# Kernel optimization log

Hardware: AMD Instinct MI355X
Metric: run time of the kernel (lower is better)

## Reference

```python
import jax, jax.numpy as jnp
import numpy as np

B, S, H, D = 8, 16, 32, 64
HID = H * D
PAST = 4096


def setup_inputs() -> dict:
    key = jax.random.key(0)
    ks = jax.random.split(key, 7)
    sc = 0.02
    return {
        "hidden_states": jax.random.normal(ks[0], (B, S, HID), jnp.float32),
        "past_k": jax.random.normal(ks[1], (B, H, PAST, D), jnp.float32),
        "past_v": jax.random.normal(ks[2], (B, H, PAST, D), jnp.float32),
        "wq": jax.random.normal(ks[3], (HID, HID), jnp.float32) * sc,
        "wk": jax.random.normal(ks[4], (HID, HID), jnp.float32) * sc,
        "wv": jax.random.normal(ks[5], (HID, HID), jnp.float32) * sc,
        "wo": jax.random.normal(ks[6], (HID, HID), jnp.float32) * sc,
    }


def reference(hidden_states, past_k, past_v, wq, wk, wv, wo):
    b, s, _ = hidden_states.shape
    # QKV projections (torch Linear: x @ W.T), split into heads -> [B,H,S,D]
    q = (hidden_states @ wq.T).reshape(b, s, H, D).transpose(0, 2, 1, 3)
    k = (hidden_states @ wk.T).reshape(b, s, H, D).transpose(0, 2, 1, 3)
    v = (hidden_states @ wv.T).reshape(b, s, H, D).transpose(0, 2, 1, 3)
    # KV-cache concat: [B,H,past+S,D]
    k = jnp.concatenate([past_k, k], axis=2)
    v = jnp.concatenate([past_v, v], axis=2)
    scale = 1.0 / jnp.sqrt(jnp.asarray(D, hidden_states.dtype))
    # scores [B,H,S,T]
    scores = jnp.einsum("bhsd,bhtd->bhst", q, k) * scale
    probs = jax.nn.softmax(scores, axis=-1)
    out = jnp.einsum("bhst,bhtd->bhsd", probs, v)
    out = out.transpose(0, 2, 1, 3).reshape(b, s, HID)
    return out @ wo.T
```

## Files before the change

kernel.cpp:

```cpp
#include <hip/hip_runtime.h>
#include <hip/hip_bf16.h>
#include <stdint.h>

#define HID 2048
#define NH  32
#define HD  64
#define NB  8
#define NS  16
#define PAST 4096

#define QSCALE 0.18033688011112042591f
#define MSTATIC 16.0f

typedef __attribute__((ext_vector_type(8))) short short8;
typedef __attribute__((ext_vector_type(4))) short short4v;
typedef __attribute__((ext_vector_type(4))) float f32x4;

#define MFMA(a, b, c) __builtin_amdgcn_mfma_f32_16x16x32_bf16((a), (b), (c), 0, 0, 0)

#define PART_STRIDE 1088
#define NSPLIT 8
#define MATSZ (128 * HID)
#define VP 68
#define WSLAB 4352

static __device__ __forceinline__ short f2bf(float f) {
    __hip_bfloat16 h = __float2bfloat16(f);
    return *reinterpret_cast<short*>(&h);
}

static __device__ __forceinline__ f32x4 ld4(const float* p) {
    return *reinterpret_cast<const f32x4*>(p);
}
static __device__ __forceinline__ f32x4 ldnt(const float* p) {
    return __builtin_nontemporal_load(reinterpret_cast<const f32x4*>(p));
}

static __device__ __forceinline__ short8 pack8(f32x4 a, f32x4 b) {
    short8 r;
    r[0] = f2bf(a[0]); r[1] = f2bf(a[1]); r[2] = f2bf(a[2]); r[3] = f2bf(a[3]);
    r[4] = f2bf(b[0]); r[5] = f2bf(b[1]); r[6] = f2bf(b[2]); r[7] = f2bf(b[3]);
    return r;
}

static __device__ __forceinline__ short4v pack4(f32x4 a) {
    short4v r;
    r[0] = f2bf(a[0]); r[1] = f2bf(a[1]); r[2] = f2bf(a[2]); r[3] = f2bf(a[3]);
    return r;
}

static __device__ __forceinline__ short8 pack8s(f32x4 a, f32x4 b, float s) {
    short8 r;
    r[0] = f2bf(a[0] * s); r[1] = f2bf(a[1] * s); r[2] = f2bf(a[2] * s); r[3] = f2bf(a[3] * s);
    r[4] = f2bf(b[0] * s); r[5] = f2bf(b[1] * s); r[6] = f2bf(b[2] * s); r[7] = f2bf(b[3] * s);
    return r;
}

__global__ __launch_bounds__(256) void cvt_kernel(const float* __restrict__ in,
                                                  short* __restrict__ out) {
    int i = (blockIdx.x * 256 + threadIdx.x) * 4;
    f32x4 v = ld4(in + i);
    *reinterpret_cast<short4v*>(out + i) = pack4(v);
}

__global__ __launch_bounds__(128) void proj_kernel(
        const short* __restrict__ X,
        const float* __restrict__ W0, const float* __restrict__ W1,
        const float* __restrict__ W2,
        float* __restrict__ Yp) {
    int mat   = blockIdx.x >> 9;
    int rest  = blockIdx.x & 511;
    int strip = rest >> 2, ks = rest & 3;
    int nbase = strip * 16;
    int k0    = ks * 512;
    const float* W = (mat == 0) ? W0 : (mat == 1) ? W1 : W2;
    float* Y = Yp + (size_t)(mat * 4 + ks) * MATSZ;

    int lane = threadIdx.x & 63;
    int wave = threadIdx.x >> 6;
    int lr = lane & 15, g = lane >> 4;

    f32x4 acc0 = {0.f, 0.f, 0.f, 0.f};
    f32x4 acc1 = {0.f, 0.f, 0.f, 0.f};
    f32x4 acc2 = {0.f, 0.f, 0.f, 0.f};
    f32x4 acc3 = {0.f, 0.f, 0.f, 0.f};

    const short* xr = X + (size_t)(wave * 64 + lr) * HID + g * 8 + k0;
    const float* wr = W + (size_t)(nbase + lr) * HID + g * 8 + k0;

    #pragma unroll 4
    for (int kc = 0; kc < 512; kc += 32) {
        f32x4 w0 = ldnt(wr + kc);
        f32x4 w1 = ldnt(wr + kc + 4);
        short8 bb = pack8(w0, w1);
        short8 a0 = *reinterpret_cast<const short8*>(xr + kc);
        short8 a1 = *reinterpret_cast<const short8*>(xr + (size_t)16 * HID + kc);
        short8 a2 = *reinterpret_cast<const short8*>(xr + (size_t)32 * HID + kc);
        short8 a3 = *reinterpret_cast<const short8*>(xr + (size_t)48 * HID + kc);
        acc0 = MFMA(a0, bb, acc0);
        acc1 = MFMA(a1, bb, acc1);
        acc2 = MFMA(a2, bb, acc2);
        acc3 = MFMA(a3, bb, acc3);
    }
    #define STACC(accv, f) do { \
        Y[(size_t)(wave * 64 + (f) * 16 + (g << 2) + 0) * HID + nbase + lr] = accv[0]; \
        Y[(size_t)(wave * 64 + (f) * 16 + (g << 2) + 1) * HID + nbase + lr] = accv[1]; \
        Y[(size_t)(wave * 64 + (f) * 16 + (g << 2) + 2) * HID + nbase + lr] = accv[2]; \
        Y[(size_t)(wave * 64 + (f) * 16 + (g << 2) + 3) * HID + nbase + lr] = accv[3]; \
    } while (0)
    STACC(acc0, 0); STACC(acc1, 1); STACC(acc2, 2); STACC(acc3, 3);
    #undef STACC
}

__global__ __launch_bounds__(256) void merge4_kernel(
        const float* __restrict__ Yp,
        float* __restrict__ Y0, float* __restrict__ Y1, float* __restrict__ Y2) {
    int mat = blockIdx.x >> 8;
    int blk = blockIdx.x & 255;
    float* Y = (mat == 0) ? Y0 : (mat == 1) ? Y1 : Y2;
    const float* P = Yp + (size_t)mat * 4 * MATSZ;
    int idx = blk * 1024 + threadIdx.x * 4;
    f32x4 a = ld4(P + idx);
    f32x4 b = ld4(P + MATSZ + idx);
    f32x4 c = ld4(P + 2 * MATSZ + idx);
    f32x4 d = ld4(P + 3 * MATSZ + idx);
    f32x4 s = a + b + c + d;
    *reinterpret_cast<f32x4*>(Y + idx) = s;
}

__global__ __launch_bounds__(256, 4) void attn_kernel(
        const float* __restrict__ q,
        const float* __restrict__ knew, const float* __restrict__ vnew,
        const float* __restrict__ pastK, const float* __restrict__ pastV,
        float* __restrict__ parts) {
    __shared__ __align__(16) unsigned char lds_raw[4 * WSLAB];
    __shared__ float s_l[4][4][16];

    int bid = blockIdx.x;
    int bh = bid >> 3, split = bid & 7;
    int b = bh >> 5, h = bh & 31;
    int wave = threadIdx.x >> 6, lane = threadIdx.x & 63;
    int lq = lane & 15, g = lane >> 4;
    int vrow = lane >> 4;
    int vcol = (lane & 15) * 4;

    unsigned short* vbuf0 = (unsigned short*)(lds_raw + wave * WSLAB);
    unsigned short* vbuf1 = vbuf0 + 16 * VP;

    const float* qp = q + (size_t)(b * NS + lq) * HID + h * HD + g * 8;
    short8 qf0, qf1;
    {
        f32x4 a0 = ld4(qp);
        f32x4 a1 = ld4(qp + 4);
        f32x4 a2 = ld4(qp + 32);
        f32x4 a3 = ld4(qp + 36);
        qf0 = pack8s(a0, a1, QSCALE);
        qf1 = pack8s(a2, a3, QSCALE);
    }

    f32x4 o0 = {0.f, 0.f, 0.f, 0.f};
    f32x4 o1 = {0.f, 0.f, 0.f, 0.f};
    f32x4 o2 = {0.f, 0.f, 0.f, 0.f};
    f32x4 o3 = {0.f, 0.f, 0.f, 0.f};
    float lsum = 0.0f;

    const float* ksplit = pastK + (size_t)bh * PAST * HD + (size_t)split * 512 * HD;
    const float* vsplit = pastV + (size_t)bh * PAST * HD + (size_t)split * 512 * HD;

    #define ISSUE_K(T, A, Bv, C, D) do { \
        const float* kr_ = ksplit + (size_t)((T) * 64 + wave * 16 + lq) * HD + (g << 3); \
        A  = ldnt(kr_); \
        Bv = ldnt(kr_ + 4); \
        C  = ldnt(kr_ + 32); \
        D  = ldnt(kr_ + 36); \
    } while (0)

    #define ISSUE_V(T, V0, V1, V2, V3) do { \
        const float* vr_ = vsplit + (size_t)((T) * 64 + wave * 16) * HD; \
        V0 = ldnt(vr_ + (0 * 4 + vrow) * HD + vcol); \
        V1 = ldnt(vr_ + (1 * 4 + vrow) * HD + vcol); \
        V2 = ldnt(vr_ + (2 * 4 + vrow) * HD + vcol); \
        V3 = ldnt(vr_ + (3 * 4 + vrow) * HD + vcol); \
    } while (0)

    #define DSW(V0, V1, V2, V3, BUFP) do { \
        unsigned short* ds_ = (BUFP); \
        *reinterpret_cast<short4v*>(ds_ + (0 * 4 + vrow) * VP + vcol) = pack4(V0); \
        *reinterpret_cast<short4v*>(ds_ + (1 * 4 + vrow) * VP + vcol) = pack4(V1); \
        *reinterpret_cast<short4v*>(ds_ + (2 * 4 + vrow) * VP + vcol) = pack4(V2); \
        *reinterpret_cast<short4v*>(ds_ + (3 * 4 + vrow) * VP + vcol) = pack4(V3); \
    } while (0)

    #define QKSM(A, Bv, C, D, PF) do { \
        short8 af0 = pack8(A, Bv); \
        short8 af1 = pack8(C, D); \
        f32x4 sv = {0.f, 0.f, 0.f, 0.f}; \
        sv = MFMA(af0, qf0, sv); \
        sv = MFMA(af1, qf1, sv); \
        float e0 = exp2f(sv[0] - MSTATIC); \
        float e1 = exp2f(sv[1] - MSTATIC); \
        float e2 = exp2f(sv[2] - MSTATIC); \
        float e3 = exp2f(sv[3] - MSTATIC); \
        lsum += e0 + e1 + e2 + e3; \
        PF[0] = f2bf(e0); PF[1] = f2bf(e1); PF[2] = f2bf(e2); PF[3] = f2bf(e3); \
        PF[4] = 0; PF[5] = 0; PF[6] = 0; PF[7] = 0; \
    } while (0)

    #define PV(BUFP, PF) do { \
        const unsigned short* vc = (BUFP) + (g << 2) * VP; \
        short8 vf; \
        vf[4] = 0; vf[5] = 0; vf[6] = 0; vf[7] = 0; \
        vf[0] = (short)vc[0 * VP + lq];      vf[1] = (short)vc[1 * VP + lq]; \
        vf[2] = (short)vc[2 * VP + lq];      vf[3] = (short)vc[3 * VP + lq]; \
        o0 = MFMA(vf, PF, o0); \
        vf[0] = (short)vc[0 * VP + 16 + lq]; vf[1] = (short)vc[1 * VP + 16 + lq]; \
        vf[2] = (short)vc[2 * VP + 16 + lq]; vf[3] = (short)vc[3 * VP + 16 + lq]; \
        o1 = MFMA(vf, PF, o1); \
        vf[0] = (short)vc[0 * VP + 32 + lq]; vf[1] = (short)vc[1 * VP + 32 + lq]; \
        vf[2] = (short)vc[2 * VP + 32 + lq]; vf[3] = (short)vc[3 * VP + 32 + lq]; \
        o2 = MFMA(vf, PF, o2); \
        vf[0] = (short)vc[0 * VP + 48 + lq]; vf[1] = (short)vc[1 * VP + 48 + lq]; \
        vf[2] = (short)vc[2 * VP + 48 + lq]; vf[3] = (short)vc[3 * VP + 48 + lq]; \
        o3 = MFMA(vf, PF, o3); \
    } while (0)

    f32x4 kA0, kA1, kA2, kA3, kB0, kB1, kB2, kB3;
    f32x4 vA0, vA1, vA2, vA3, vB0, vB1, vB2, vB3;

    ISSUE_V(0, vA0, vA1, vA2, vA3);
    ISSUE_K(0, kA0, kA1, kA2, kA3);
    DSW(vA0, vA1, vA2, vA3, vbuf0);
    ISSUE_V(1, vB0, vB1, vB2, vB3);
    ISSUE_K(1, kB0, kB1, kB2, kB3);

    #pragma unroll 1
    for (int tt = 0; tt < 4; ++tt) {
        short8 pfE;
        QKSM(kA0, kA1, kA2, kA3, pfE);
        DSW(vB0, vB1, vB2, vB3, vbuf1);
        if (tt < 3) {
            ISSUE_V(2 * tt + 2, vA0, vA1, vA2, vA3);
            ISSUE_K(2 * tt + 2, kA0, kA1, kA2, kA3);
        }
        PV(vbuf0, pfE);
        short8 pfO;
        QKSM(kB0, kB1, kB2, kB3, pfO);
        if (tt < 3) {
            DSW(vA0, vA1, vA2, vA3, vbuf0);
            ISSUE_V(2 * tt + 3, vB0, vB1, vB2, vB3);
            ISSUE_K(2 * tt + 3, kB0, kB1, kB2, kB3);
        }
        PV(vbuf1, pfO);
    }
    #undef PV
    #undef QKSM
    #undef DSW
    #undef ISSUE_V
    #undef ISSUE_K

    if (split == 0 && wave == 0) {
        const float* kr = knew + (size_t)(b * NS + lq) * HID + h * HD + g * 8;
        f32x4 ka = ld4(kr);
        f32x4 kb2 = ld4(kr + 4);
        f32x4 kc2 = ld4(kr + 32);
        f32x4 kd2 = ld4(kr + 36);
        short8 af0 = pack8(ka, kb2);
        short8 af1 = pack8(kc2, kd2);
        f32x4 sv = {0.f, 0.f, 0.f, 0.f};
        sv = MFMA(af0, qf0, sv);
        sv = MFMA(af1, qf1, sv);

        float e0 = exp2f(sv[0] - MSTATIC);
        float e1 = exp2f(sv[1] - MSTATIC);
        float e2 = exp2f(sv[2] - MSTATIC);
        float e3 = exp2f(sv[3] - MSTATIC);
        lsum += e0 + e1 + e2 + e3;

        short8 pfT;
        pfT[0] = f2bf(e0); pfT[1] = f2bf(e1); pfT[2] = f2bf(e2); pfT[3] = f2bf(e3);
        pfT[4] = 0; pfT[5] = 0; pfT[6] = 0; pfT[7] = 0;

        const float* vt2 = vnew + (size_t)(b * NS) * HID + h * HD;
        #define LOADVT(dst, dcol) do { \
            dst[0] = f2bf(vt2[(size_t)((g << 2) + 0) * HID + (dcol)]); \
            dst[1] = f2bf(vt2[(size_t)((g << 2) + 1) * HID + (dcol)]); \
            dst[2] = f2bf(vt2[(size_t)((g << 2) + 2) * HID + (dcol)]); \
            dst[3] = f2bf(vt2[(size_t)((g << 2) + 3) * HID + (dcol)]); \
            dst[4] = 0; dst[5] = 0; dst[6] = 0; dst[7] = 0; \
        } while (0)
        short8 vv0, vv1, vv2, vv3;
        LOADVT(vv0, lq); LOADVT(vv1, 16 + lq); LOADVT(vv2, 32 + lq); LOADVT(vv3, 48 + lq);
        #undef LOADVT
        o0 = MFMA(vv0, pfT, o0);
        o1 = MFMA(vv1, pfT, o1);
        o2 = MFMA(vv2, pfT, o2);
        o3 = MFMA(vv3, pfT, o3);
    }

    float* so_w = (float*)(lds_raw + wave * WSLAB);
    #define STO(ov, dt) do { \
        so_w[lq * 64 + (dt) * 16 + (g << 2) + 0] = ov[0]; \
        so_w[lq * 64 + (dt) * 16 + (g << 2) + 1] = ov[1]; \
        so_w[lq * 64 + (dt) * 16 + (g << 2) + 2] = ov[2]; \
        so_w[lq * 64 + (dt) * 16 + (g << 2) + 3] = ov[3]; \
    } while (0)
    STO(o0, 0); STO(o1, 1); STO(o2, 2); STO(o3, 3);
    #undef STO
    s_l[wave][g][lq] = lsum;
    __syncthreads();

    if (wave == 0) {
        float L = 0.f;
        #pragma unroll
        for (int w = 0; w < 4; ++w)
            L += s_l[w][0][lq] + s_l[w][1][lq] + s_l[w][2][lq] + s_l[w][3][lq];
        const float* so0 = (const float*)(lds_raw + 0 * WSLAB);
        const float* so1 = (const float*)(lds_raw + 1 * WSLAB);
        const float* so2 = (const float*)(lds_raw + 2 * WSLAB);
        const float* so3 = (const float*)(lds_raw + 3 * WSLAB);
        float* pbase = parts + (size_t)bid * PART_STRIDE;
        if (g == 0) pbase[lq] = L;
        for (int dd = 0; dd < 16; ++dd) {
            int di = g * 16 + dd;
            float v = so0[lq * 64 + di] + so1[lq * 64 + di] +
                      so2[lq * 64 + di] + so3[lq * 64 + di];
            pbase[32 + lq * 64 + di] = v;
        }
    }
}

__global__ __launch_bounds__(256) void merge_kernel(const float* __restrict__ parts,
                                                    short* __restrict__ attnb) {
    int bh = blockIdx.x;
    int tid = threadIdx.x;
    int qi = tid >> 4, ds = (tid & 15) * 4;
    const float* pb0 = parts + (size_t)(bh * NSPLIT) * PART_STRIDE;

    float L = 0.f;
    #pragma unroll
    for (int i = 0; i < NSPLIT; ++i)
        L += pb0[(size_t)i * PART_STRIDE + qi];
    float inv = 1.0f / L;

    int b = bh >> 5, h = bh & 31;
    int base = 32 + qi * 64 + ds;
    short4v o;
    #pragma unroll
    for (int r = 0; r < 4; ++r) {
        float v = pb0[(size_t)0 * PART_STRIDE + base + r]
                + pb0[(size_t)1 * PART_STRIDE + base + r]
                + pb0[(size_t)2 * PART_STRIDE + base + r]
                + pb0[(size_t)3 * PART_STRIDE + base + r]
                + pb0[(size_t)4 * PART_STRIDE + base + r]
                + pb0[(size_t)5 * PART_STRIDE + base + r]
                + pb0[(size_t)6 * PART_STRIDE + base + r]
                + pb0[(size_t)7 * PART_STRIDE + base + r];
        o[r] = f2bf(v * inv);
    }
    *reinterpret_cast<short4v*>(attnb + (size_t)(b * NS + qi) * HID + h * HD + ds) = o;
}

extern "C" void kernel_launch(void* const* d_in, const int* in_sizes, int n_in,
                              void* d_out, int out_size, void* d_ws, size_t ws_size,
                              hipStream_t stream) {
    const float* hs     = (const float*)d_in[0];
    const float* past_k = (const float*)d_in[1];
    const float* past_v = (const float*)d_in[2];
    const float* wq     = (const float*)d_in[3];
    const float* wk     = (const float*)d_in[4];
    const float* wv     = (const float*)d_in[5];
    const float* wo     = (const float*)d_in[6];
    float* out = (float*)d_out;

    float* qb    = (float*)d_ws;
    float* kn    = qb + MATSZ;
    float* vn    = kn + MATSZ;
    short* hsb   = (short*)(vn + MATSZ);
    short* attnb = hsb + MATSZ;
    float* parts = (float*)(attnb + MATSZ);
    float* qkvp  = parts + 2048 * PART_STRIDE;
    float* op    = qkvp + 3 * 4 * MATSZ;

    cvt_kernel<<<256, 256, 0, stream>>>(hs, hsb);
    proj_kernel<<<1536, 128, 0, stream>>>(hsb, wq, wk, wv, qkvp);
    merge4_kernel<<<768, 256, 0, stream>>>(qkvp, qb, kn, vn);
    attn_kernel<<<256 * NSPLIT, 256, 0, stream>>>(qb, kn, vn, past_k, past_v, parts);
    merge_kernel<<<256, 256, 0, stream>>>(parts, attnb);
    proj_kernel<<<512, 128, 0, stream>>>(attnb, wo, wo, wo, op);
    merge4_kernel<<<256, 256, 0, stream>>>(op, out, out, out);
}
```

Measured before the change: 183.3 us.

## Drop split-KV, stream K/V via global_load_lds triple buffer, fuse merge

The attention kernel now runs one block per (batch, head) instead of eight KV splits. Each wave streams K and V tiles straight into swizzled LDS with global_load_lds and keeps a three-slot ring paced by explicit vmcnt waits. The final normalization is written directly as bf16, which removes the partials buffer and the separate merge kernel launch. The cost is only 256 blocks on a large GPU, which lowers parallelism and memory-level concurrency, and each block now walks the whole 4096-token sequence.

Result: faster. 171.9 us (-6.2%).

```diff
diff --git a/kernel.cpp b/kernel.cpp
--- a/kernel.cpp
+++ b/kernel.cpp
@@ -18,11 +18,11 @@
 
 #define MFMA(a, b, c) __builtin_amdgcn_mfma_f32_16x16x32_bf16((a), (b), (c), 0, 0, 0)
 
-#define PART_STRIDE 1088
-#define NSPLIT 8
 #define MATSZ (128 * HID)
-#define VP 68
-#define WSLAB 4352
+#define SLOTB 32768
+#define SW16(r, cb) ((cb) ^ (((r) & 7) << 4))
+#define VMCNT(N) asm volatile("s_waitcnt vmcnt(" #N ")" ::: "memory")
+#define SB0 __builtin_amdgcn_sched_barrier(0)
 
 static __device__ __forceinline__ short f2bf(float f) {
     __hip_bfloat16 h = __float2bfloat16(f);
@@ -34,6 +34,13 @@
 }
 static __device__ __forceinline__ f32x4 ldnt(const float* p) {
     return __builtin_nontemporal_load(reinterpret_cast<const f32x4*>(p));
+}
+
+static __device__ __forceinline__ void gl16(const char* g, char* l) {
+    __builtin_amdgcn_global_load_lds(
+        (const __attribute__((address_space(1))) void*)(g),
+        (__attribute__((address_space(3))) void*)(l),
+        16, 0, 0);
 }
 
 static __device__ __forceinline__ short8 pack8(f32x4 a, f32x4 b) {
@@ -128,24 +135,20 @@
     *reinterpret_cast<f32x4*>(Y + idx) = s;
 }
 
-__global__ __launch_bounds__(256, 4) void attn_kernel(
+__global__ __launch_bounds__(256) void attn_kernel(
         const float* __restrict__ q,
         const float* __restrict__ knew, const float* __restrict__ vnew,
         const float* __restrict__ pastK, const float* __restrict__ pastV,
-        float* __restrict__ parts) {
-    __shared__ __align__(16) unsigned char lds_raw[4 * WSLAB];
-    __shared__ float s_l[4][4][16];
-
-    int bid = blockIdx.x;
-    int bh = bid >> 3, split = bid & 7;
+        short* __restrict__ attnb) {
+    __shared__ __align__(16) unsigned char lds_raw[3 * SLOTB];
+    __shared__ float s_l2[4][4][16];
+
+    int bh = blockIdx.x;
     int b = bh >> 5, h = bh & 31;
     int wave = threadIdx.x >> 6, lane = threadIdx.x & 63;
     int lq = lane & 15, g = lane >> 4;
-    int vrow = lane >> 4;
-    int vcol = (lane & 15) * 4;
-
-    unsigned short* vbuf0 = (unsigned short*)(lds_raw + wave * WSLAB);
-    unsigned short* vbuf1 = vbuf0 + 16 * VP;
+    int rl = lane >> 4;
+    int cbl = (lane & 15) * 16;
 
     const float* qp = q + (size_t)(b * NS + lq) * HID + h * HD + g * 8;
     short8 qf0, qf1;
@@ -157,6 +160,7 @@
         qf0 = pack8s(a0, a1, QSCALE);
         qf1 = pack8s(a2, a3, QSCALE);
     }
+    SB0;
 
     f32x4 o0 = {0.f, 0.f, 0.f, 0.f};
     f32x4 o1 = {0.f, 0.f, 0.f, 0.f};
@@ -164,36 +168,35 @@
     f32x4 o3 = {0.f, 0.f, 0.f, 0.f};
     float lsum = 0.0f;
 
-    const float* ksplit = pastK + (size_t)bh * PAST * HD + (size_t)split * 512 * HD;
-    const float* vsplit = pastV + (size_t)bh * PAST * HD + (size_t)split * 512 * HD;
-
-    #define ISSUE_K(T, A, Bv, C, D) do { \
-        const float* kr_ = ksplit + (size_t)((T) * 64 + wave * 16 + lq) * HD + (g << 3); \
-        A  = ldnt(kr_); \
-        Bv = ldnt(kr_ + 4); \
-        C  = ldnt(kr_ + 32); \
-        D  = ldnt(kr_ + 36); \
+    const char* kbh = (const char*)(pastK + (size_t)bh * PAST * HD);
+    const char* vbh = (const char*)(pastV + (size_t)bh * PAST * HD);
+
+    #define ISSUE(T, S) do { \
+        const char* kg_ = kbh + (size_t)((T) * 64 + wave * 16) * 256; \
+        const char* vg_ = vbh + (size_t)((T) * 64 + wave * 16) * 256; \
+        char* kd_ = (char*)lds_raw + (S) * SLOTB + wave * 4096; \
+        char* vd_ = kd_ + 16384; \
+        gl16(kg_ + ((0 + rl) * 256 + SW16((0 + rl), cbl)),   kd_ + 0 * 1024 + lane * 16); \
+        gl16(kg_ + ((4 + rl) * 256 + SW16((4 + rl), cbl)),   kd_ + 1 * 1024 + lane * 16); \
+        gl16(kg_ + ((8 + rl) * 256 + SW16((8 + rl), cbl)),   kd_ + 2 * 1024 + lane * 16); \
+        gl16(kg_ + ((12 + rl) * 256 + SW16((12 + rl), cbl)), kd_ + 3 * 1024 + lane * 16); \
+        gl16(vg_ + ((0 + rl) * 256 + SW16((0 + rl), cbl)),   vd_ + 0 * 1024 + lane * 16); \
+        gl16(vg_ + ((4 + rl) * 256 + SW16((4 + rl), cbl)),   vd_ + 1 * 1024 + lane * 16); \
+        gl16(vg_ + ((8 + rl) * 256 + SW16((8 + rl), cbl)),   vd_ + 2 * 1024 + lane * 16); \
+        gl16(vg_ + ((12 + rl) * 256 + SW16((12 + rl), cbl)), vd_ + 3 * 1024 + lane * 16); \
     } while (0)
 
-    #define ISSUE_V(T, V0, V1, V2, V3) do { \
-        const float* vr_ = vsplit + (size_t)((T) * 64 + wave * 16) * HD; \
-        V0 = ldnt(vr_ + (0 * 4 + vrow) * HD + vcol); \
-        V1 = ldnt(vr_ + (1 * 4 + vrow) * HD + vcol); \
-        V2 = ldnt(vr_ + (2 * 4 + vrow) * HD + vcol); \
-        V3 = ldnt(vr_ + (3 * 4 + vrow) * HD + vcol); \
-    } while (0)
-
-    #define DSW(V0, V1, V2, V3, BUFP) do { \
-        unsigned short* ds_ = (BUFP); \
-        *reinterpret_cast<short4v*>(ds_ + (0 * 4 + vrow) * VP + vcol) = pack4(V0); \
-        *reinterpret_cast<short4v*>(ds_ + (1 * 4 + vrow) * VP + vcol) = pack4(V1); \
-        *reinterpret_cast<short4v*>(ds_ + (2 * 4 + vrow) * VP + vcol) = pack4(V2); \
-        *reinterpret_cast<short4v*>(ds_ + (3 * 4 + vrow) * VP + vcol) = pack4(V3); \
-    } while (0)
-
-    #define QKSM(A, Bv, C, D, PF) do { \
-        short8 af0 = pack8(A, Bv); \
-        short8 af1 = pack8(C, D); \
+    #define LVF(vb, r, dc) (*(const float*)((vb) + (r) * 256 + (((dc) * 4) ^ (((r) & 7) << 4))))
+
+    #define TILEC(S) do { \
+        const char* kb_ = (const char*)lds_raw + (S) * SLOTB + wave * 4096; \
+        const char* vb_ = kb_ + 16384; \
+        f32x4 a0 = *(const f32x4*)(kb_ + lq * 256 + SW16(lq, g * 32)); \
+        f32x4 a1 = *(const f32x4*)(kb_ + lq * 256 + SW16(lq, g * 32 + 16)); \
+        f32x4 a2 = *(const f32x4*)(kb_ + lq * 256 + SW16(lq, 128 + g * 32)); \
+        f32x4 a3 = *(const f32x4*)(kb_ + lq * 256 + SW16(lq, 128 + g * 32 + 16)); \
+        short8 af0 = pack8(a0, a1); \
+        short8 af1 = pack8(a2, a3); \
         f32x4 sv = {0.f, 0.f, 0.f, 0.f}; \
         sv = MFMA(af0, qf0, sv); \
         sv = MFMA(af1, qf1, sv); \
@@ -202,63 +205,43 @@
         float e2 = exp2f(sv[2] - MSTATIC); \
         float e3 = exp2f(sv[3] - MSTATIC); \
         lsum += e0 + e1 + e2 + e3; \
-        PF[0] = f2bf(e0); PF[1] = f2bf(e1); PF[2] = f2bf(e2); PF[3] = f2bf(e3); \
-        PF[4] = 0; PF[5] = 0; PF[6] = 0; PF[7] = 0; \
-    } while (0)
-
-    #define PV(BUFP, PF) do { \
-        const unsigned short* vc = (BUFP) + (g << 2) * VP; \
+        short8 pf; \
+        pf[0] = f2bf(e0); pf[1] = f2bf(e1); pf[2] = f2bf(e2); pf[3] = f2bf(e3); \
+        pf[4] = 0; pf[5] = 0; pf[6] = 0; pf[7] = 0; \
+        int r0 = g << 2; \
         short8 vf; \
         vf[4] = 0; vf[5] = 0; vf[6] = 0; vf[7] = 0; \
-        vf[0] = (short)vc[0 * VP + lq];      vf[1] = (short)vc[1 * VP + lq]; \
-        vf[2] = (short)vc[2 * VP + lq];      vf[3] = (short)vc[3 * VP + lq]; \
-        o0 = MFMA(vf, PF, o0); \
-        vf[0] = (short)vc[0 * VP + 16 + lq]; vf[1] = (short)vc[1 * VP + 16 + lq]; \
-        vf[2] = (short)vc[2 * VP + 16 + lq]; vf[3] = (short)vc[3 * VP + 16 + lq]; \
-        o1 = MFMA(vf, PF, o1); \
-        vf[0] = (short)vc[0 * VP + 32 + lq]; vf[1] = (short)vc[1 * VP + 32 + lq]; \
-        vf[2] = (short)vc[2 * VP + 32 + lq]; vf[3] = (short)vc[3 * VP + 32 + lq]; \
-        o2 = MFMA(vf, PF, o2); \
-        vf[0] = (short)vc[0 * VP + 48 + lq]; vf[1] = (short)vc[1 * VP + 48 + lq]; \
-        vf[2] = (short)vc[2 * VP + 48 + lq]; vf[3] = (short)vc[3 * VP + 48 + lq]; \
-        o3 = MFMA(vf, PF, o3); \
+        vf[0] = f2bf(LVF(vb_, r0 + 0, lq));      vf[1] = f2bf(LVF(vb_, r0 + 1, lq)); \
+        vf[2] = f2bf(LVF(vb_, r0 + 2, lq));      vf[3] = f2bf(LVF(vb_, r0 + 3, lq)); \
+        o0 = MFMA(vf, pf, o0); \
+        vf[0] = f2bf(LVF(vb_, r0 + 0, 16 + lq)); vf[1] = f2bf(LVF(vb_, r0 + 1, 16 + lq)); \
+        vf[2] = f2bf(LVF(vb_, r0 + 2, 16 + lq)); vf[3] = f2bf(LVF(vb_, r0 + 3, 16 + lq)); \
+        o1 = MFMA(vf, pf, o1); \
+        vf[0] = f2bf(LVF(vb_, r0 + 0, 32 + lq)); vf[1] = f2bf(LVF(vb_, r0 + 1, 32 + lq)); \
+        vf[2] = f2bf(LVF(vb_, r0 + 2, 32 + lq)); vf[3] = f2bf(LVF(vb_, r0 + 3, 32 + lq)); \
+        o2 = MFMA(vf, pf, o2); \
+        vf[0] = f2bf(LVF(vb_, r0 + 0, 48 + lq)); vf[1] = f2bf(LVF(vb_, r0 + 1, 48 + lq)); \
+        vf[2] = f2bf(LVF(vb_, r0 + 2, 48 + lq)); vf[3] = f2bf(LVF(vb_, r0 + 3, 48 + lq)); \
+        o3 = MFMA(vf, pf, o3); \
     } while (0)
 
-    f32x4 kA0, kA1, kA2, kA3, kB0, kB1, kB2, kB3;
-    f32x4 vA0, vA1, vA2, vA3, vB0, vB1, vB2, vB3;
-
-    ISSUE_V(0, vA0, vA1, vA2, vA3);
-    ISSUE_K(0, kA0, kA1, kA2, kA3);
-    DSW(vA0, vA1, vA2, vA3, vbuf0);
-    ISSUE_V(1, vB0, vB1, vB2, vB3);
-    ISSUE_K(1, kB0, kB1, kB2, kB3);
+    ISSUE(0, 0); ISSUE(1, 1); ISSUE(2, 2);
 
     #pragma unroll 1
-    for (int tt = 0; tt < 4; ++tt) {
-        short8 pfE;
-        QKSM(kA0, kA1, kA2, kA3, pfE);
-        DSW(vB0, vB1, vB2, vB3, vbuf1);
-        if (tt < 3) {
-            ISSUE_V(2 * tt + 2, vA0, vA1, vA2, vA3);
-            ISSUE_K(2 * tt + 2, kA0, kA1, kA2, kA3);
-        }
-        PV(vbuf0, pfE);
-        short8 pfO;
-        QKSM(kB0, kB1, kB2, kB3, pfO);
-        if (tt < 3) {
-            DSW(vA0, vA1, vA2, vA3, vbuf0);
-            ISSUE_V(2 * tt + 3, vB0, vB1, vB2, vB3);
-            ISSUE_K(2 * tt + 3, kB0, kB1, kB2, kB3);
-        }
-        PV(vbuf1, pfO);
-    }
-    #undef PV
-    #undef QKSM
-    #undef DSW
-    #undef ISSUE_V
-    #undef ISSUE_K
-
-    if (split == 0 && wave == 0) {
+    for (int it = 0; it < 20; ++it) {
+        int t = it * 3;
+        VMCNT(16); SB0; TILEC(0); ISSUE(t + 3, 0);
+        VMCNT(16); SB0; TILEC(1); ISSUE(t + 4, 1);
+        VMCNT(16); SB0; TILEC(2); ISSUE(t + 5, 2);
+    }
+    VMCNT(16); SB0; TILEC(0); ISSUE(63, 0);
+    VMCNT(16); SB0; TILEC(1);
+    VMCNT(8);  SB0; TILEC(2);
+    VMCNT(0);  SB0; TILEC(0);
+    #undef TILEC
+    #undef ISSUE
+
+    if (wave == 0) {
         const float* kr = knew + (size_t)(b * NS + lq) * HID + h * HD + g * 8;
         f32x4 ka = ld4(kr);
         f32x4 kb2 = ld4(kr + 4);
@@ -297,7 +280,7 @@
         o3 = MFMA(vv3, pfT, o3);
     }
 
-    float* so_w = (float*)(lds_raw + wave * WSLAB);
+    float* so_w = (float*)(lds_raw + wave * 4096);
     #define STO(ov, dt) do { \
         so_w[lq * 64 + (dt) * 16 + (g << 2) + 0] = ov[0]; \
         so_w[lq * 64 + (dt) * 16 + (g << 2) + 1] = ov[1]; \
@@ -306,58 +289,28 @@
     } while (0)
     STO(o0, 0); STO(o1, 1); STO(o2, 2); STO(o3, 3);
     #undef STO
-    s_l[wave][g][lq] = lsum;
+    s_l2[wave][g][lq] = lsum;
     __syncthreads();
 
     if (wave == 0) {
         float L = 0.f;
         #pragma unroll
         for (int w = 0; w < 4; ++w)
-            L += s_l[w][0][lq] + s_l[w][1][lq] + s_l[w][2][lq] + s_l[w][3][lq];
-        const float* so0 = (const float*)(lds_raw + 0 * WSLAB);
-        const float* so1 = (const float*)(lds_raw + 1 * WSLAB);
-        const float* so2 = (const float*)(lds_raw + 2 * WSLAB);
-        const float* so3 = (const float*)(lds_raw + 3 * WSLAB);
-        float* pbase = parts + (size_t)bid * PART_STRIDE;
-        if (g == 0) pbase[lq] = L;
+            L += s_l2[w][0][lq] + s_l2[w][1][lq] + s_l2[w][2][lq] + s_l2[w][3][lq];
+        float inv = 1.0f / L;
+        const float* so0 = (const float*)(lds_raw + 0 * 4096);
+        const float* so1 = (const float*)(lds_raw + 1 * 4096);
+        const float* so2 = (const float*)(lds_raw + 2 * 4096);
+        const float* so3 = (const float*)(lds_raw + 3 * 4096);
+        short* op = attnb + (size_t)(b * NS + lq) * HID + h * HD + g * 16;
+        #pragma unroll
         for (int dd = 0; dd < 16; ++dd) {
             int di = g * 16 + dd;
             float v = so0[lq * 64 + di] + so1[lq * 64 + di] +
                       so2[lq * 64 + di] + so3[lq * 64 + di];
-            pbase[32 + lq * 64 + di] = v;
+            op[dd] = f2bf(v * inv);
         }
     }
-}
-
-__global__ __launch_bounds__(256) void merge_kernel(const float* __restrict__ parts,
-                                                    short* __restrict__ attnb) {
-    int bh = blockIdx.x;
-    int tid = threadIdx.x;
-    int qi = tid >> 4, ds = (tid & 15) * 4;
-    const float* pb0 = parts + (size_t)(bh * NSPLIT) * PART_STRIDE;
-
-    float L = 0.f;
-    #pragma unroll
-    for (int i = 0; i < NSPLIT; ++i)
-        L += pb0[(size_t)i * PART_STRIDE + qi];
-    float inv = 1.0f / L;
-
-    int b = bh >> 5, h = bh & 31;
-    int base = 32 + qi * 64 + ds;
-    short4v o;
-    #pragma unroll
-    for (int r = 0; r < 4; ++r) {
-        float v = pb0[(size_t)0 * PART_STRIDE + base + r]
-                + pb0[(size_t)1 * PART_STRIDE + base + r]
-                + pb0[(size_t)2 * PART_STRIDE + base + r]
-                + pb0[(size_t)3 * PART_STRIDE + base + r]
-                + pb0[(size_t)4 * PART_STRIDE + base + r]
-                + pb0[(size_t)5 * PART_STRIDE + base + r]
-                + pb0[(size_t)6 * PART_STRIDE + base + r]
-                + pb0[(size_t)7 * PART_STRIDE + base + r];
-        o[r] = f2bf(v * inv);
-    }
-    *reinterpret_cast<short4v*>(attnb + (size_t)(b * NS + qi) * HID + h * HD + ds) = o;
 }
 
 extern "C" void kernel_launch(void* const* d_in, const int* in_sizes, int n_in,
@@ -377,15 +330,13 @@
     float* vn    = kn + MATSZ;
     short* hsb   = (short*)(vn + MATSZ);
     short* attnb = hsb + MATSZ;
-    float* parts = (float*)(attnb + MATSZ);
-    float* qkvp  = parts + 2048 * PART_STRIDE;
+    float* qkvp  = (float*)(attnb + MATSZ);
     float* op    = qkvp + 3 * 4 * MATSZ;
 
     cvt_kernel<<<256, 256, 0, stream>>>(hs, hsb);
     proj_kernel<<<1536, 128, 0, stream>>>(hsb, wq, wk, wv, qkvp);
     merge4_kernel<<<768, 256, 0, stream>>>(qkvp, qb, kn, vn);
-    attn_kernel<<<256 * NSPLIT, 256, 0, stream>>>(qb, kn, vn, past_k, past_v, parts);
-    merge_kernel<<<256, 256, 0, stream>>>(parts, attnb);
+    attn_kernel<<<256, 256, 0, stream>>>(qb, kn, vn, past_k, past_v, attnb);
     proj_kernel<<<512, 128, 0, stream>>>(attnb, wo, wo, wo, op);
     merge4_kernel<<<256, 256, 0, stream>>>(op, out, out, out);
 }
```
